# Optimization experiments

Hardware: AMD Instinct MI355X
Metric: run time of the kernel (lower is better)

The kernel has to match this reference:

```python
import jax, jax.numpy as jnp
import numpy as np

H = 12          # num attention heads
D = 768         # hidden size
DH = D // H     # head dim = 64

def setup_inputs() -> dict:
    key = jax.random.key(0)
    ks = jax.random.split(key, 9)
    B, N = 8, 1024
    s = 0.02
    return {
        "hidden_states": jax.random.normal(ks[0], (B, N, D), jnp.float32),
        "Wq": jax.random.normal(ks[1], (D, D), jnp.float32) * s,
        "bq": jnp.zeros((D,), jnp.float32),
        "Wk": jax.random.normal(ks[2], (D, D), jnp.float32) * s,
        "bk": jnp.zeros((D,), jnp.float32),
        "Wv": jax.random.normal(ks[3], (D, D), jnp.float32) * s,
        "bv": jnp.zeros((D,), jnp.float32),
        "Wo": jax.random.normal(ks[4], (D, D), jnp.float32) * s,
        "bo": jnp.zeros((D,), jnp.float32),
    }

def _split_heads(x):
    # [B, N, D] -> [B, H, N, DH]
    B, N, _ = x.shape
    return x.reshape(B, N, H, DH).transpose(0, 2, 1, 3)

def reference(hidden_states, Wq, bq, Wk, bk, Wv, bv, Wo, bo):
    # torch Linear: y = x @ W.T + b
    q = _split_heads(hidden_states @ Wq.T + bq)
    k = _split_heads(hidden_states @ Wk.T + bk)
    v = _split_heads(hidden_states @ Wv.T + bv)
    scale = 1.0 / jnp.sqrt(jnp.asarray(DH, hidden_states.dtype))
    scores = jnp.einsum("bhqd,bhkd->bhqk", q, k) * scale
    probs = jax.nn.softmax(scores, axis=-1)
    ctx = jnp.einsum("bhqk,bhkd->bhqd", probs, v)
    B, _, N, _ = ctx.shape
    ctx = ctx.transpose(0, 2, 1, 3).reshape(B, N, D)
    return ctx @ Wo.T + bo
```

## Files before the change

kernel.cpp:

```cpp
#include <hip/hip_runtime.h>

typedef unsigned short u16;
typedef unsigned int   u32;
typedef unsigned long long u64;
typedef __attribute__((ext_vector_type(8))) short bf16x8;
typedef __attribute__((ext_vector_type(4))) float f32x4;
typedef __attribute__((address_space(3))) u32 lds_u32;
typedef __attribute__((address_space(1))) u32 gbl_u32;

#define MFMA16(a,b,c) __builtin_amdgcn_mfma_f32_16x16x32_bf16((a),(b),(c),0,0,0)
#define QSCALE 0.1803368801111204f

#define WAIT4 do{ asm volatile("s_waitcnt vmcnt(4)" ::: "memory"); }while(0)
#define WAIT0 do{ asm volatile("s_waitcnt vmcnt(0)" ::: "memory"); }while(0)
#define SCHED __builtin_amdgcn_sched_barrier(0)
#define BARR  __builtin_amdgcn_s_barrier()

__device__ __forceinline__ u16 f2bf(float f){
  u32 u = __builtin_bit_cast(u32, f);
  u32 r = u + 0x7fffu + ((u>>16)&1u);
  return (u16)(r>>16);
}
__device__ __forceinline__ float bf2f(u16 h){
  return __builtin_bit_cast(float, (u32)h<<16);
}

union V8 { u16 s[8]; uint4 v; };

__global__ __launch_bounds__(256) void cvt_all(const float* __restrict__ hs,
    const float* __restrict__ Wq, const float* __restrict__ Wk,
    const float* __restrict__ Wv, const float* __restrict__ Wo,
    u16* __restrict__ hsb, u16* __restrict__ wqkv, u16* __restrict__ woh)
{
  const int bid = blockIdx.x;
  if (bid < 3072){
    int i = bid*256 + threadIdx.x;
    const float4* p = (const float4*)(hs + (size_t)i*8);
    float4 a = p[0], b = p[1];
    V8 t;
    t.s[0]=f2bf(a.x); t.s[1]=f2bf(a.y); t.s[2]=f2bf(a.z); t.s[3]=f2bf(a.w);
    t.s[4]=f2bf(b.x); t.s[5]=f2bf(b.y); t.s[6]=f2bf(b.z); t.s[7]=f2bf(b.w);
    *(uint4*)(hsb + (size_t)i*8) = t.v;
    return;
  }
  const int r = bid - 3072;
  const int seg = r / 288;
  const int off = (r - seg*288)*256 + threadIdx.x;
  const float* src = seg==0?Wq: seg==1?Wk: seg==2?Wv: Wo;
  const float4* p = (const float4*)(src + (size_t)off*8);
  float4 a = p[0], b = p[1];
  float xs[8] = {a.x,a.y,a.z,a.w,b.x,b.y,b.z,b.w};
  V8 t;
  #pragma unroll
  for (int j=0;j<8;++j) t.s[j]=f2bf(xs[j]);
  if (seg < 3) *(uint4*)(wqkv + (size_t)seg*589824 + (size_t)off*8) = t.v;
  else         *(uint4*)(woh  + (size_t)off*8) = t.v;
}

__global__ __launch_bounds__(256) void mm_qkv(const u16* __restrict__ A, const u16* __restrict__ Bp,
    const float* __restrict__ bq, const float* __restrict__ bk, const float* __restrict__ bvv,
    u16* __restrict__ Oq, u16* __restrict__ Ok, u16* __restrict__ Ov)
{
  __shared__ u16 P[3][8192];
  const int bid = blockIdx.x;
  const int sid = (bid & 7)*144 + (bid >> 3);
  const int mb = sid/18, nb = sid - mb*18;
  const int m0 = mb*128, n0 = nb*128;
  const int tid = threadIdx.x;
  const int lane = tid&63, wid = tid>>6;
  const int wr = wid>>1, wc = wid&1;
  const int fr = lane&15, fg = lane>>4;

  const char* Ab = (const char*)A;
  const char* Bb = (const char*)Bp;
  const char* sp[4];
  #pragma unroll
  for (int c=0;c<4;++c){
    int ci = c*256 + tid;
    int row = ci>>3, slot = ci&7;
    int d = slot ^ (row&7);
    if (d < 4) sp[c] = Ab + (size_t)(m0+row)*1536 + d*16;
    else       sp[c] = Bb + (size_t)(n0+row)*1536 + (d-4)*16;
  }
  const int sA = (fg ^ (fr&7)) << 4;
  const int sB = sA ^ 64;

  f32x4 zz = {0.f,0.f,0.f,0.f};
  f32x4 acc[4][4];
  #pragma unroll
  for (int i=0;i<4;++i)
    #pragma unroll
    for (int j=0;j<4;++j) acc[i][j]=zz;

  auto STAGE = [&](int t, int b){
    char* dst0 = (char*)P[b];
    #pragma unroll
    for (int c=0;c<4;++c)
      __builtin_amdgcn_global_load_lds((const gbl_u32*)(sp[c] + (size_t)t*64),
        (lds_u32*)(dst0 + c*4096 + wid*1024), 16, 0, 0);
  };
  auto COMPUTE = [&](int b){
    const char* pb = (const char*)P[b];
    bf16x8 bfr[4];
    #pragma unroll
    for (int nt=0;nt<4;++nt)
      bfr[nt] = *(const bf16x8*)(pb + (wc*64+nt*16+fr)*128 + sB);
    #pragma unroll
    for (int mt=0;mt<4;++mt){
      bf16x8 af = *(const bf16x8*)(pb + (wr*64+mt*16+fr)*128 + sA);
      #pragma unroll
      for (int nt=0;nt<4;++nt)
        acc[mt][nt] = MFMA16(af, bfr[nt], acc[mt][nt]);
    }
  };

  STAGE(0, 0); STAGE(1, 1);
  int cb = 0;
  for (int t=0; t<24; ++t){
    if (t < 23) WAIT4; else WAIT0;
    BARR; SCHED;
    if (t < 22){
      int sb = cb + 2; if (sb >= 3) sb -= 3;
      STAGE(t+2, sb);
    }
    __builtin_amdgcn_s_setprio(1);
    COMPUTE(cb);
    __builtin_amdgcn_s_setprio(0);
    cb = (cb == 2) ? 0 : cb + 1;
  }

  const int seg = nb/6;
  const float* bias = seg==0?bq: seg==1?bk:bvv;
  const float sc = (seg==0) ? QSCALE : 1.0f;
  if (seg < 2){
    u16* O = seg==0?Oq:Ok;
    #pragma unroll
    for (int mt=0;mt<4;++mt){
      #pragma unroll
      for (int nt=0;nt<4;++nt){
        int colw = n0 + wc*64 + nt*16 + fr - seg*768;
        float bz = bias[colw];
        int hh = colw>>6, d = colw&63;
        #pragma unroll
        for (int rr=0;rr<4;++rr){
          int row = m0 + wr*64 + mt*16 + fg*4 + rr;
          int b = row>>10, nn = row&1023;
          O[((size_t)(b*12+hh)<<16) + (size_t)nn*64 + d] = f2bf((acc[mt][nt][rr] + bz) * sc);
        }
      }
    }
  } else {
    #pragma unroll
    for (int mt=0;mt<4;++mt){
      #pragma unroll
      for (int nt=0;nt<4;++nt){
        int colw = n0 + wc*64 + nt*16 + fr - 1536;
        float bz = bias[colw];
        int hh = colw>>6, d = colw&63;
        int row0 = m0 + wr*64 + mt*16 + fg*4;
        int b = row0>>10, nn = row0&1023;
        union { u16 h[4]; u64 q; } pk;
        #pragma unroll
        for (int rr=0;rr<4;++rr) pk.h[rr] = f2bf(acc[mt][nt][rr] + bz);
        *(u64*)&Ov[((size_t)(b*12+hh)<<16) + (size_t)d*1024 + nn] = pk.q;
      }
    }
  }
}

__global__ __launch_bounds__(256) void mm_o(const u16* __restrict__ A, const u16* __restrict__ Bp,
                                            const float* __restrict__ bias, float* __restrict__ O)
{
  __shared__ u16 P[3][8192];
  const int bid = blockIdx.x;
  const int sid = (bid & 7)*48 + (bid >> 3);
  const int mb = sid/6, nb = sid - mb*6;
  const int m0 = mb*128, n0 = nb*128;
  const int tid = threadIdx.x;
  const int lane = tid&63, wid = tid>>6;
  const int wr = wid>>1, wc = wid&1;
  const int fr = lane&15, fg = lane>>4;

  const char* Ab = (const char*)A;
  const char* Bb = (const char*)Bp;
  const char* sp[4];
  #pragma unroll
  for (int c=0;c<4;++c){
    int ci = c*256 + tid;
    int row = ci>>3, slot = ci&7;
    int d = slot ^ (row&7);
    if (d < 4) sp[c] = Ab + (size_t)(m0+row)*1536 + d*16;
    else       sp[c] = Bb + (size_t)(n0+row)*1536 + (d-4)*16;
  }
  const int sA = (fg ^ (fr&7)) << 4;
  const int sB = sA ^ 64;

  f32x4 zz = {0.f,0.f,0.f,0.f};
  f32x4 acc[4][4];
  #pragma unroll
  for (int i=0;i<4;++i)
    #pragma unroll
    for (int j=0;j<4;++j) acc[i][j]=zz;

  auto STAGE = [&](int t, int b){
    char* dst0 = (char*)P[b];
    #pragma unroll
    for (int c=0;c<4;++c)
      __builtin_amdgcn_global_load_lds((const gbl_u32*)(sp[c] + (size_t)t*64),
        (lds_u32*)(dst0 + c*4096 + wid*1024), 16, 0, 0);
  };
  auto COMPUTE = [&](int b){
    const char* pb = (const char*)P[b];
    bf16x8 bfr[4];
    #pragma unroll
    for (int nt=0;nt<4;++nt)
      bfr[nt] = *(const bf16x8*)(pb + (wc*64+nt*16+fr)*128 + sB);
    #pragma unroll
    for (int mt=0;mt<4;++mt){
      bf16x8 af = *(const bf16x8*)(pb + (wr*64+mt*16+fr)*128 + sA);
      #pragma unroll
      for (int nt=0;nt<4;++nt)
        acc[mt][nt] = MFMA16(af, bfr[nt], acc[mt][nt]);
    }
  };

  STAGE(0, 0); STAGE(1, 1);
  int cb = 0;
  for (int t=0; t<24; ++t){
    if (t < 23) WAIT4; else WAIT0;
    BARR; SCHED;
    if (t < 22){
      int sb = cb + 2; if (sb >= 3) sb -= 3;
      STAGE(t+2, sb);
    }
    __builtin_amdgcn_s_setprio(1);
    COMPUTE(cb);
    __builtin_amdgcn_s_setprio(0);
    cb = (cb == 2) ? 0 : cb + 1;
  }

  #pragma unroll
  for (int mt=0;mt<4;++mt){
    #pragma unroll
    for (int nt=0;nt<4;++nt){
      int colb = n0 + wc*64 + nt*16 + fr;
      float bz = bias[colb];
      #pragma unroll
      for (int rr=0;rr<4;++rr){
        int row = m0 + wr*64 + mt*16 + fg*4 + rr;
        O[(size_t)row*768 + colb] = acc[mt][nt][rr] + bz;
      }
    }
  }
}

__global__ __launch_bounds__(256) void attn(const u16* __restrict__ qh, const u16* __restrict__ kh,
                                            const u16* __restrict__ vh, u16* __restrict__ ch)
{
  __shared__ u16 Kb[2][4096];
  __shared__ u16 Vb[2][4096];
  __shared__ u16 Ps[4][32][72];
  const int tid=threadIdx.x, w=tid>>6, lane=tid&63;
  const int fr=lane&15, fg=lane>>4;
  const int bh=blockIdx.x, qt=blockIdx.y;
  const size_t base=(size_t)bh<<16;
  const int q0=qt*128 + w*32;

  const char* kbase = (const char*)(kh + base);
  const char* vbase = (const char*)(vh + base);

  int koff[2], voff[2];
  #pragma unroll
  for (int c=0;c<2;++c){
    int ci = c*256 + tid;
    int row = ci>>3;
    int colp = ((ci&7)*16) ^ ((row&7)<<4);
    koff[c] = row*128  + colp;
    voff[c] = row*2048 + colp;
  }

  bf16x8 qf[2][2];
  #pragma unroll
  for (int mt=0;mt<2;++mt)
    #pragma unroll
    for (int ks=0;ks<2;++ks)
      qf[mt][ks] = *(const bf16x8*)&qh[base + (size_t)(q0+mt*16+fr)*64 + ks*32 + fg*8];

  const int swz = (fr&7)<<4;
  int lowD[2];
  #pragma unroll
  for (int ks=0;ks<2;++ks) lowD[ks] = (ks*64 + fg*16) ^ swz;
  const int frbase = fr*128;

  f32x4 zz = {0.f,0.f,0.f,0.f};
  f32x4 o[2][4];
  float lr[2][4];
  #pragma unroll
  for (int mt=0;mt<2;++mt)
    #pragma unroll
    for (int j=0;j<4;++j){ o[mt][j]=zz; lr[mt][j]=0.f; }

  {
    #pragma unroll
    for (int c=0;c<2;++c){
      __builtin_amdgcn_global_load_lds((const gbl_u32*)(kbase + koff[c]),
        (lds_u32*)((char*)&Kb[0][0] + c*4096 + w*1024), 16, 0, 0);
      __builtin_amdgcn_global_load_lds((const gbl_u32*)(vbase + voff[c]),
        (lds_u32*)((char*)&Vb[0][0] + c*4096 + w*1024), 16, 0, 0);
    }
  }
  __syncthreads();

  for (int kt=0; kt<16; ++kt){
    const int buf = kt & 1;
    {
      const int ktn = (kt+1) & 15;
      const char* kt_ = kbase + ktn*8192;
      const char* vt_ = vbase + ktn*128;
      #pragma unroll
      for (int c=0;c<2;++c){
        __builtin_amdgcn_global_load_lds((const gbl_u32*)(kt_ + koff[c]),
          (lds_u32*)((char*)&Kb[buf^1][0] + c*4096 + w*1024), 16, 0, 0);
        __builtin_amdgcn_global_load_lds((const gbl_u32*)(vt_ + voff[c]),
          (lds_u32*)((char*)&Vb[buf^1][0] + c*4096 + w*1024), 16, 0, 0);
      }
    }

    f32x4 s[2][4];
    #pragma unroll
    for (int mt=0;mt<2;++mt)
      #pragma unroll
      for (int j=0;j<4;++j) s[mt][j]=zz;
    const char* kb = (const char*)&Kb[buf][0];
    __builtin_amdgcn_s_setprio(1);
    #pragma unroll
    for (int ct=0;ct<4;++ct){
      #pragma unroll
      for (int ks=0;ks<2;++ks){
        bf16x8 kf = *(const bf16x8*)(kb + ct*2048 + frbase + lowD[ks]);
        s[0][ct]=MFMA16(qf[0][ks],kf,s[0][ct]);
        s[1][ct]=MFMA16(qf[1][ks],kf,s[1][ct]);
      }
    }
    __builtin_amdgcn_s_setprio(0);

    #pragma unroll
    for (int mt=0;mt<2;++mt){
      #pragma unroll
      for (int rr=0;rr<4;++rr){
        int qr = mt*16+fg*4+rr;
        float acc_l = 0.f;
        #pragma unroll
        for (int ct=0;ct<4;++ct){
          float e = __builtin_amdgcn_exp2f(s[mt][ct][rr]);
          u32 u = __builtin_bit_cast(u32, e);
          acc_l += __builtin_bit_cast(float, u & 0xffff0000u);
          Ps[w][qr][ct*16+fr] = (u16)(u>>16);
        }
        lr[mt][rr] += acc_l;
      }
    }

    const char* vb = (const char*)&Vb[buf][0];
    __builtin_amdgcn_s_setprio(1);
    #pragma unroll
    for (int ks2=0;ks2<2;++ks2){
      bf16x8 vf[4];
      #pragma unroll
      for (int dt=0;dt<4;++dt)
        vf[dt] = *(const bf16x8*)(vb + dt*2048 + frbase + lowD[ks2]);
      #pragma unroll
      for (int mt=0;mt<2;++mt){
        bf16x8 pa = *(const bf16x8*)&Ps[w][mt*16+fr][ks2*32+fg*8];
        #pragma unroll
        for (int dt=0;dt<4;++dt)
          o[mt][dt]=MFMA16(pa, vf[dt], o[mt][dt]);
      }
    }
    __builtin_amdgcn_s_setprio(0);

    __syncthreads();
  }

  float inv[2][4];
  #pragma unroll
  for (int mt=0;mt<2;++mt)
    #pragma unroll
    for (int rr=0;rr<4;++rr){
      float l = lr[mt][rr];
      l += __shfl_xor(l,1); l += __shfl_xor(l,2);
      l += __shfl_xor(l,4); l += __shfl_xor(l,8);
      inv[mt][rr] = 1.0f / l;
    }
  const int b=bh/12, hd=bh%12;
  #pragma unroll
  for (int mt=0;mt<2;++mt){
    #pragma unroll
    for (int dt=0;dt<4;++dt){
      int d = dt*16 + fr;
      #pragma unroll
      for (int rr=0;rr<4;++rr){
        int n = q0 + mt*16 + fg*4 + rr;
        ch[((size_t)b*1024 + n)*768 + hd*64 + d] = f2bf(o[mt][dt][rr] * inv[mt][rr]);
      }
    }
  }
}

extern "C" void kernel_launch(void* const* d_in, const int* in_sizes, int n_in,
                              void* d_out, int out_size, void* d_ws, size_t ws_size,
                              hipStream_t stream) {
  const float* hs = (const float*)d_in[0];
  const float* Wq = (const float*)d_in[1];
  const float* bq = (const float*)d_in[2];
  const float* Wk = (const float*)d_in[3];
  const float* bk = (const float*)d_in[4];
  const float* Wv = (const float*)d_in[5];
  const float* bv = (const float*)d_in[6];
  const float* Wo = (const float*)d_in[7];
  const float* bo = (const float*)d_in[8];
  float* out = (float*)d_out;

  const size_t PS = (size_t)8192*768;
  u16* ws16  = (u16*)d_ws;
  u16* hs_bf = ws16;
  u16* q_bf  = ws16 + PS;
  u16* k_bf  = ws16 + 2*PS;
  u16* v_bf  = ws16 + 3*PS;
  u16* wqkv  = ws16 + 4*PS;
  u16* woh   = wqkv + 3*589824;
  u16* c_hi  = hs_bf;

  dim3 blk(256);
  cvt_all<<<3072 + 4*288, blk, 0, stream>>>(hs, Wq, Wk, Wv, Wo, hs_bf, wqkv, woh);
  mm_qkv<<<1152, blk, 0, stream>>>(hs_bf, wqkv, bq, bk, bv, q_bf, k_bf, v_bf);
  attn<<<dim3(96,8), blk, 0, stream>>>(q_bf, k_bf, v_bf, c_hi);
  mm_o<<<384, blk, 0, stream>>>(c_hi, woh, bo, out);
}
```

Before: 119.5 us.

## Widen QKV GEMM tile to 128x256 with 8 waves and new LDS layout

Result: no change. 118.8 us (-0.6%).

```diff
diff --git a/kernel.cpp b/kernel.cpp
--- a/kernel.cpp
+++ b/kernel.cpp
@@ -11,6 +11,7 @@
 #define MFMA16(a,b,c) __builtin_amdgcn_mfma_f32_16x16x32_bf16((a),(b),(c),0,0,0)
 #define QSCALE 0.1803368801111204f
 
+#define WAIT3 do{ asm volatile("s_waitcnt vmcnt(3)" ::: "memory"); }while(0)
 #define WAIT4 do{ asm volatile("s_waitcnt vmcnt(4)" ::: "memory"); }while(0)
 #define WAIT0 do{ asm volatile("s_waitcnt vmcnt(0)" ::: "memory"); }while(0)
 #define SCHED __builtin_amdgcn_sched_barrier(0)
@@ -57,33 +58,42 @@
   else         *(uint4*)(woh  + (size_t)off*8) = t.v;
 }
 
-__global__ __launch_bounds__(256) void mm_qkv(const u16* __restrict__ A, const u16* __restrict__ Bp,
+__global__ __launch_bounds__(512) void mm_qkv(const u16* __restrict__ A, const u16* __restrict__ Bp,
     const float* __restrict__ bq, const float* __restrict__ bk, const float* __restrict__ bvv,
     u16* __restrict__ Oq, u16* __restrict__ Ok, u16* __restrict__ Ov)
 {
-  __shared__ u16 P[3][8192];
+  __shared__ u16 P[3][12288];
   const int bid = blockIdx.x;
-  const int sid = (bid & 7)*144 + (bid >> 3);
-  const int mb = sid/18, nb = sid - mb*18;
-  const int m0 = mb*128, n0 = nb*128;
+  const int sid = (bid & 7)*72 + (bid >> 3);
+  const int mb = sid/9, nb = sid - mb*9;
+  const int m0 = mb*128, n0 = nb*256;
   const int tid = threadIdx.x;
   const int lane = tid&63, wid = tid>>6;
-  const int wr = wid>>1, wc = wid&1;
+  const int wr = wid>>2, wc = wid&3;
   const int fr = lane&15, fg = lane>>4;
 
   const char* Ab = (const char*)A;
   const char* Bb = (const char*)Bp;
-  const char* sp[4];
-  #pragma unroll
-  for (int c=0;c<4;++c){
-    int ci = c*256 + tid;
-    int row = ci>>3, slot = ci&7;
-    int d = slot ^ (row&7);
-    if (d < 4) sp[c] = Ab + (size_t)(m0+row)*1536 + d*16;
-    else       sp[c] = Bb + (size_t)(n0+row)*1536 + (d-4)*16;
-  }
-  const int sA = (fg ^ (fr&7)) << 4;
-  const int sB = sA ^ 64;
+  const char* sp[3];
+  #pragma unroll
+  for (int c=0;c<3;++c){
+    int ci = c*512 + tid;
+    if (ci < 512){
+      int line = ci>>3, slot = ci&7;
+      int d = slot ^ (line&7);
+      int row = 2*line + (d>>2);
+      sp[c] = Ab + (size_t)(m0+row)*1536 + (d&3)*16;
+    } else {
+      int i = ci - 512;
+      int line = i>>3, slot = i&7;
+      int d = slot ^ (line&7);
+      int row = 2*line + (d>>2);
+      sp[c] = Bb + (size_t)(n0+row)*1536 + (d&3)*16;
+    }
+  }
+  const int sl = (((fr&1)<<2) + fg) ^ (fr>>1);
+  const int aoff = (fr&~1)*64 + sl*16 + wr*4096;
+  const int boff = 8192 + (fr&~1)*64 + sl*16 + wc*4096;
 
   f32x4 zz = {0.f,0.f,0.f,0.f};
   f32x4 acc[4][4];
@@ -95,19 +105,19 @@
   auto STAGE = [&](int t, int b){
     char* dst0 = (char*)P[b];
     #pragma unroll
-    for (int c=0;c<4;++c)
+    for (int c=0;c<3;++c)
       __builtin_amdgcn_global_load_lds((const gbl_u32*)(sp[c] + (size_t)t*64),
-        (lds_u32*)(dst0 + c*4096 + wid*1024), 16, 0, 0);
+        (lds_u32*)(dst0 + c*8192 + wid*1024), 16, 0, 0);
   };
   auto COMPUTE = [&](int b){
     const char* pb = (const char*)P[b];
     bf16x8 bfr[4];
     #pragma unroll
     for (int nt=0;nt<4;++nt)
-      bfr[nt] = *(const bf16x8*)(pb + (wc*64+nt*16+fr)*128 + sB);
+      bfr[nt] = *(const bf16x8*)(pb + boff + nt*1024);
     #pragma unroll
     for (int mt=0;mt<4;++mt){
-      bf16x8 af = *(const bf16x8*)(pb + (wr*64+mt*16+fr)*128 + sA);
+      bf16x8 af = *(const bf16x8*)(pb + aoff + mt*1024);
       #pragma unroll
       for (int nt=0;nt<4;++nt)
         acc[mt][nt] = MFMA16(af, bfr[nt], acc[mt][nt]);
@@ -117,7 +127,7 @@
   STAGE(0, 0); STAGE(1, 1);
   int cb = 0;
   for (int t=0; t<24; ++t){
-    if (t < 23) WAIT4; else WAIT0;
+    if (t < 23) WAIT3; else WAIT0;
     BARR; SCHED;
     if (t < 22){
       int sb = cb + 2; if (sb >= 3) sb -= 3;
@@ -129,7 +139,7 @@
     cb = (cb == 2) ? 0 : cb + 1;
   }
 
-  const int seg = nb/6;
+  const int seg = nb/3;
   const float* bias = seg==0?bq: seg==1?bk:bvv;
   const float sc = (seg==0) ? QSCALE : 1.0f;
   if (seg < 2){
@@ -433,7 +443,7 @@
 
   dim3 blk(256);
   cvt_all<<<3072 + 4*288, blk, 0, stream>>>(hs, Wq, Wk, Wv, Wo, hs_bf, wqkv, woh);
-  mm_qkv<<<1152, blk, 0, stream>>>(hs_bf, wqkv, bq, bk, bv, q_bf, k_bf, v_bf);
+  mm_qkv<<<576, dim3(512), 0, stream>>>(hs_bf, wqkv, bq, bk, bv, q_bf, k_bf, v_bf);
   attn<<<dim3(96,8), blk, 0, stream>>>(q_bf, k_bf, v_bf, c_hi);
   mm_o<<<384, blk, 0, stream>>>(c_hi, woh, bo, out);
 }
```
